# Performance work log

Hardware: AMD Instinct MI355X
Metric: run time of the kernel (lower is better)

Reference implementation:

```python
import jax, jax.numpy as jnp
import numpy as np

NDIM = 128
GDIM = 128
NUM_LAYERS = 2
B = 8192
IDX = 16          # nodes per graph
EPG = 32          # edges per graph
N = B * IDX       # total nodes = 131072
E = B * EPG       # total edges = 262144


def setup_inputs() -> dict:
    key = jax.random.key(0)
    ks = jax.random.split(key, 24)
    h = jax.random.normal(ks[0], (B, IDX, NDIM), dtype=jnp.float32)
    # edges constrained within each graph (flattened node indexing)
    gid = jnp.repeat(jnp.arange(B, dtype=jnp.int64), EPG)
    src = gid * IDX + jax.random.randint(ks[1], (E,), 0, IDX).astype(jnp.int64)
    dst = gid * IDX + jax.random.randint(ks[2], (E,), 0, IDX).astype(jnp.int64)
    edge_index = jnp.stack([src, dst], axis=0)
    s = 0.05
    inp = {
        'h': h,
        'edge_index': edge_index,
        'msg_W': jax.random.normal(ks[3], (NUM_LAYERS, 2 * NDIM, 2 * NDIM), jnp.float32) * s,
        'msg_b': jax.random.normal(ks[4], (NUM_LAYERS, 2 * NDIM), jnp.float32) * s,
        'msgr_W': jax.random.normal(ks[5], (NUM_LAYERS, 2 * NDIM, 2 * NDIM), jnp.float32) * s,
        'msgr_b': jax.random.normal(ks[6], (NUM_LAYERS, 2 * NDIM), jnp.float32) * s,
        'gru_Wih': jax.random.normal(ks[7], (NUM_LAYERS, 3 * NDIM, 2 * NDIM), jnp.float32) * s,
        'gru_Whh': jax.random.normal(ks[8], (NUM_LAYERS, 3 * NDIM, NDIM), jnp.float32) * s,
        'gru_bih': jax.random.normal(ks[9], (NUM_LAYERS, 3 * NDIM), jnp.float32) * s,
        'gru_bhh': jax.random.normal(ks[10], (NUM_LAYERS, 3 * NDIM), jnp.float32) * s,
        'fm_W': jax.random.normal(ks[11], (GDIM, NDIM), jnp.float32) * s,
        'fm_b': jax.random.normal(ks[12], (GDIM,), jnp.float32) * s,
        'gm_W': jax.random.normal(ks[13], (1, NDIM), jnp.float32) * s,
        'gm_b': jax.random.normal(ks[14], (1,), jnp.float32) * s,
        'fmi_W': jax.random.normal(ks[15], (GDIM, NDIM), jnp.float32) * s,
        'fmi_b': jax.random.normal(ks[16], (GDIM,), jnp.float32) * s,
        'gmi_W': jax.random.normal(ks[17], (1, NDIM), jnp.float32) * s,
        'gmi_b': jax.random.normal(ks[18], (1,), jnp.float32) * s,
    }
    return inp


def _gnn_forward(h, edge_index, msg_W, msg_b, msgr_W, msgr_b,
                 gru_Wih, gru_Whh, gru_bih, gru_bhh):
    # h: [N, ndim]; edge_index: [2, E] -> doubled with reversed edges -> [2, 2E]
    ei = jnp.concatenate([edge_index, edge_index[::-1]], axis=1)
    src, dst = ei[0], ei[1]
    e = edge_index.shape[1]
    n_nodes = h.shape[0]
    for l in range(NUM_LAYERS):
        # (eval mode: dropout p=0.0 is a no-op)
        h_j = h[src]                       # [2E, ndim]
        h_i = h[dst]                       # [2E, ndim]
        m = jnp.concatenate([h_j, h_i], axis=1)   # [2E, 2*ndim]
        m_fwd, m_rev = m[:e], m[e:]
        a = jnp.concatenate([
            m_fwd @ msg_W[l].T + msg_b[l],
            m_rev @ msgr_W[l].T + msgr_b[l],
        ], axis=0)                          # [2E, 2*ndim]
        aggr = jax.ops.segment_sum(a, dst, num_segments=n_nodes)  # [N, 2*ndim]
        # GRUCell(aggr, h): gate order r, z, n (torch convention)
        gi = aggr @ gru_Wih[l].T + gru_bih[l]   # [N, 3*ndim]
        gh = h @ gru_Whh[l].T + gru_bhh[l]      # [N, 3*ndim]
        gi_r, gi_z, gi_n = jnp.split(gi, 3, axis=1)
        gh_r, gh_z, gh_n = jnp.split(gh, 3, axis=1)
        r = jax.nn.sigmoid(gi_r + gh_r)
        z = jax.nn.sigmoid(gi_z + gh_z)
        n = jnp.tanh(gi_n + r * gh_n)
        h = n + z * (h - n)                 # (1-z)*n + z*h
    return h


def _graph_aggr(h, idx, f_W, f_b, g_W, g_b):
    # gated sum aggregation
    h_vG = h @ f_W.T + f_b                      # [N, gdim]
    g_vG = jax.nn.sigmoid(h @ g_W.T + g_b)      # [N, 1]
    out = (h_vG * g_vG).reshape(-1, idx, f_W.shape[0])
    return out.sum(axis=1)                      # [B, gdim]


def reference(h, edge_index, msg_W, msg_b, msgr_W, msgr_b,
              gru_Wih, gru_Whh, gru_bih, gru_bhh,
              fm_W, fm_b, gm_W, gm_b, fmi_W, fmi_b, gmi_W, gmi_b):
    idx = h.shape[1]
    hf = h.reshape(-1, NDIM)
    hf = _gnn_forward(hf, edge_index, msg_W, msg_b, msgr_W, msgr_b,
                      gru_Wih, gru_Whh, gru_bih, gru_bhh)
    h_G = _graph_aggr(hf, idx, fm_W, fm_b, gm_W, gm_b)
    h_G_init = _graph_aggr(hf, idx, fmi_W, fmi_b, gmi_W, gmi_b)
    return (hf.reshape(-1, idx, NDIM), h_G, h_G_init)
```

## Files before the change

kernel.cpp:

```cpp
#include <hip/hip_runtime.h>
#include <math.h>
#include <stdint.h>

#define NDIM 128
#define B_GRAPHS 8192
#define IDX 16
#define EPG 32
#define NN (B_GRAPHS*IDX)
#define NE (B_GRAPHS*EPG)

typedef short bf16x8 __attribute__((ext_vector_type(8)));
typedef float f32x4  __attribute__((ext_vector_type(4)));

__device__ inline unsigned short f2bf(float x) {
    union { float f; unsigned u; } v; v.f = x;
    unsigned r = v.u + 0x7fff + ((v.u >> 16) & 1);
    return (unsigned short)(r >> 16);
}
__device__ inline float bf2f(unsigned short b) {
    union { unsigned u; float f; } v; v.u = ((unsigned)b) << 16;
    return v.f;
}
__device__ inline float sigm(float x) { return 1.f/(1.f + __expf(-x)); }
__device__ inline float tanh_f(float x) {
    float ax = fabsf(x);
    float t  = __expf(-2.f*ax);
    float r  = (1.f - t)/(1.f + t);
    return copysignf(r, x);
}

#define GLOAD_LDS16(g, l) \
    __builtin_amdgcn_global_load_lds( \
        (const __attribute__((address_space(1))) unsigned int*)(g), \
        (__attribute__((address_space(3))) unsigned int*)(l), 16, 0, 0)

__global__ __launch_bounds__(256) void compose_kernel(
    const float* __restrict__ msg_W, const float* __restrict__ msgr_W,
    const float* __restrict__ Wih,   const float* __restrict__ Whh,
    const float* __restrict__ msg_b, const float* __restrict__ msgr_b,
    unsigned short* __restrict__ WB, float* __restrict__ c34)
{
    int idx = blockIdx.x*256 + threadIdx.x;
    const int TWB = 2*512*640;
    if (idx < TWB) {
        int l = idx / (512*640); int rem = idx - l*(512*640);
        int cold = rem / 640; int k = rem - cold*640;
        float val;
        if (k < 512) {
            if (cold < 384) {
                const float* wih = Wih + l*384*256 + cold*256;
                const float* M; int sc;
                if (k < 128)      { M = msg_W  + l*256*256; sc = k;       }
                else if (k < 256) { M = msgr_W + l*256*256; sc = k - 128; }
                else if (k < 384) { M = msg_W  + l*256*256; sc = k - 128; }
                else              { M = msgr_W + l*256*256; sc = k - 256; }
                float acc = 0.f;
                for (int q = 0; q < 256; q++) acc = fmaf(wih[q], M[q*256 + sc], acc);
                val = acc;
            } else val = 0.f;
        } else {
            int kk = k - 512;
            if (cold < 256)      val = Whh[l*384*128 + cold*128 + kk];
            else if (cold < 384) val = 0.f;
            else                 val = Whh[l*384*128 + (cold-128)*128 + kk];
        }
        int cc = cold & 127, t = cold >> 7;
        int colp = ((cc >> 4) << 6) + (t << 4) + (cc & 15);
        WB[l*512*640 + colp*640 + k] = f2bf(val);
    } else if (idx < TWB + 2*2*384) {
        int i2 = idx - TWB;
        int l = i2 / 768; int rem = i2 - l*768;
        int which = rem / 384; int r = rem - which*384;
        const float* wih = Wih + l*384*256 + r*256;
        const float* bb  = (which ? msgr_b : msg_b) + l*256;
        float acc = 0.f;
        for (int q = 0; q < 256; q++) acc = fmaf(wih[q], bb[q], acc);
        c34[l*768 + which*384 + r] = acc;
    }
}

__global__ __launch_bounds__(128) void init_kernel(
    const float* __restrict__ hin, const int* __restrict__ ei,
    unsigned short* __restrict__ A, float* __restrict__ indeg,
    float* __restrict__ outdeg, unsigned char* __restrict__ pack)
{
    int g = blockIdx.x, t = threadIdx.x;
    __shared__ float hb[16][128];
    __shared__ float sin_[16][128];
    __shared__ float sout_[16][128];
    __shared__ int sl[32], dl[32];
    __shared__ int cin[16], cout[16];
    __shared__ int flag64;
    int base = g*IDX;
    for (int r = 0; r < 16; r++) hb[r][t] = hin[(size_t)(base+r)*128 + t];
    for (int r = 0; r < 16; r++) { sin_[r][t] = 0.f; sout_[r][t] = 0.f; }
    if (t < 16) { cin[t] = 0; cout[t] = 0; }
    if (t == 0) {
        int orv = 0;
        for (int i = 1; i < 64; i += 2) orv |= ei[i];
        flag64 = (orv == 0);
    }
    __syncthreads();
    if (t < 32) {
        int e = g*EPG + t;
        int sv, dv;
        if (flag64) { sv = ei[2*e]; dv = ei[2*(NE + e)]; }
        else        { sv = ei[e];   dv = ei[NE + e];     }
        sl[t] = sv - base; dl[t] = dv - base;
        atomicAdd(&cout[sl[t]], 1); atomicAdd(&cin[dl[t]], 1);
        pack[g*32 + t] = (unsigned char)((sl[t] & 15) | ((dl[t] & 15) << 4));
    }
    __syncthreads();
    for (int e = 0; e < 32; e++) {
        sin_[dl[e]][t]  += hb[sl[e]][t];
        sout_[sl[e]][t] += hb[dl[e]][t];
    }
    for (int r = 0; r < 16; r++) {
        size_t v = base + r;
        float di = (float)cin[r], dof = (float)cout[r];
        A[v*640 + t]        = f2bf(sin_[r][t]);
        A[v*640 + 128 + t]  = f2bf(sout_[r][t]);
        A[v*640 + 256 + t]  = f2bf(di  * hb[r][t]);
        A[v*640 + 384 + t]  = f2bf(dof * hb[r][t]);
        A[v*640 + 512 + t]  = f2bf(hb[r][t]);
    }
    if (t < 16) { indeg[base+t] = (float)cin[t]; outdeg[base+t] = (float)cout[t]; }
}

struct FSmem {
    unsigned short As[2][64*64];
    union {
        unsigned short Bs[2][384*32];
        unsigned short hnewB[64*128];
    } u;
    unsigned char csr[4][2][17];
    unsigned char adj[4][2][32];
    unsigned char offj[4][2][16];
    float gates[2][64];
};

#define MF(a,b,c) __builtin_amdgcn_mfma_f32_16x16x32_bf16((a),(b),(c),0,0,0)

#define CSTEP(BB, AB, E, J2) do {                                             \
    const unsigned short* Asb = sm.As[AB];                                    \
    const unsigned short* Bsb = sm.u.Bs[BB];                                  \
    bf16x8 bfv[3];                                                            \
    _Pragma("unroll")                                                         \
    for (int tt = 0; tt < 3; tt++) {                                          \
        int a0 = wid*48 + tt*16 + l15;                                        \
        bfv[tt] = *(const bf16x8*)(Bsb + a0*32 + (l4 ^ ((a0>>1)&3))*8);       \
    }                                                                         \
    bf16x8 afv[4];                                                            \
    _Pragma("unroll")                                                         \
    for (int mi = 0; mi < 4; mi++) {                                          \
        int row = mi*16 + l15;                                                \
        int slot = ((E)*4 + l4) ^ (row & 7);                                  \
        afv[mi] = *(const bf16x8*)(Asb + row*64 + slot*8);                    \
    }                                                                         \
    __builtin_amdgcn_s_setprio(1);                                            \
    _Pragma("unroll")                                                         \
    for (int mi = 0; mi < 4; mi++) {                                          \
        acc[mi][0]  = MF(afv[mi], bfv[0], acc[mi][0]);                        \
        acc[mi][1]  = MF(afv[mi], bfv[1], acc[mi][1]);                        \
        acc[mi][J2] = MF(afv[mi], bfv[2], acc[mi][J2]);                       \
    }                                                                         \
    __builtin_amdgcn_s_setprio(0);                                            \
} while (0)

#define WB0 asm volatile("s_waitcnt vmcnt(0)\n\ts_barrier" ::: "memory")
#define WB1 asm volatile("s_waitcnt vmcnt(1)\n\ts_barrier" ::: "memory")

template <bool FINAL>
__global__ __launch_bounds__(512, 4) void fused_kernel(
    unsigned short* __restrict__ A,
    const unsigned short* __restrict__ WBl,
    const unsigned char* __restrict__ pack,
    const float* __restrict__ c34l,
    const float* __restrict__ bihl, const float* __restrict__ bhhl,
    const float* __restrict__ gmW,  const float* __restrict__ gmb,
    const float* __restrict__ gmiW, const float* __restrict__ gmib,
    float* __restrict__ hf, float* __restrict__ P1, float* __restrict__ P2,
    float* __restrict__ sg)
{
    __shared__ FSmem sm;
    const int n0  = blockIdx.x * 64;
    const int g0  = blockIdx.x * 4;
    const int tid = threadIdx.x;
    const int lane = tid & 63, wid = tid >> 6;
    const int l15 = lane & 15, l4 = lane >> 4;

    const int arow = tid >> 3;
    const unsigned short* Abase =
        A + (size_t)(n0 + arow)*640 + (size_t)(((tid & 7) ^ (arow & 7)) * 8);
    int boffv[3], baddv[3];
#pragma unroll
    for (int i = 0; i < 3; i++) {
        int u = i*512 + tid;
        int a = u >> 2, s = u & 3;
        int grp = a / 48, rem = a - grp*48;
        int tt = rem >> 4, clo = rem & 15;
        boffv[i] = (grp*64 + tt*16 + clo)*640 + (s ^ ((a >> 1) & 3))*8;
        baddv[i] = (tt == 2) ? 16*640 : 0;
    }

    auto STAGE_A2 = [&](int p) {
        GLOAD_LDS16(Abase + p*64, sm.As[p & 1] + tid*8);
    };
    auto STAGE_B = [&](int kst) {
        unsigned short* dst = sm.u.Bs[kst & 1] + tid*8;
        const unsigned short* srcb = WBl + kst*32;
        if (kst < 16) {
#pragma unroll
            for (int i = 0; i < 3; i++)
                GLOAD_LDS16(srcb + boffv[i], dst + i*4096);
        } else {
#pragma unroll
            for (int i = 0; i < 3; i++)
                GLOAD_LDS16(srcb + boffv[i] + baddv[i], dst + i*4096);
        }
    };

    STAGE_B(0); STAGE_A2(0);
    if (tid < 8) {
        int gl = tid >> 1, dir = tid & 1;
        const unsigned char* pk = pack + (size_t)(g0 + gl)*32;
        unsigned char* C = sm.csr[gl][dir];
        for (int d = 0; d < 17; d++) C[d] = 0;
        for (int e = 0; e < 32; e++) {
            int p = pk[e];
            int key = dir ? (p & 15) : (p >> 4);
            C[key + 1]++;
        }
        for (int d = 0; d < 16; d++) { C[d+1] += C[d]; sm.offj[gl][dir][d] = C[d]; }
        for (int e = 0; e < 32; e++) {
            int p = pk[e];
            int key = dir ? (p & 15) : (p >> 4);
            int val = dir ? (p >> 4) : (p & 15);
            sm.adj[gl][dir][sm.offj[gl][dir][key]++] = val;
        }
    }

    f32x4 acc[4][4] = {};

    WB0;
    STAGE_B(1);  STAGE_A2(1); CSTEP(0, 0, 0, 2);
    WB1; STAGE_B(2);          CSTEP(1, 0, 1, 2);
    WB0; STAGE_B(3);  STAGE_A2(2); CSTEP(0, 1, 0, 2);
    WB1; STAGE_B(4);          CSTEP(1, 1, 1, 2);
    WB0; STAGE_B(5);  STAGE_A2(3); CSTEP(0, 0, 0, 2);
    WB1; STAGE_B(6);          CSTEP(1, 0, 1, 2);
    WB0; STAGE_B(7);  STAGE_A2(4); CSTEP(0, 1, 0, 2);
    WB1; STAGE_B(8);          CSTEP(1, 1, 1, 2);
    WB0; STAGE_B(9);  STAGE_A2(5); CSTEP(0, 0, 0, 2);
    WB1; STAGE_B(10);         CSTEP(1, 0, 1, 2);
    WB0; STAGE_B(11); STAGE_A2(6); CSTEP(0, 1, 0, 2);
    WB1; STAGE_B(12);         CSTEP(1, 1, 1, 2);
    WB0; STAGE_B(13); STAGE_A2(7); CSTEP(0, 0, 0, 2);
    WB1; STAGE_B(14);         CSTEP(1, 0, 1, 2);
    WB0; STAGE_B(15); STAGE_A2(8); CSTEP(0, 1, 0, 2);
    WB1; STAGE_B(16);         CSTEP(1, 1, 1, 2);
    WB0; STAGE_B(17); STAGE_A2(9); CSTEP(0, 0, 0, 3);
    WB1; STAGE_B(18);         CSTEP(1, 0, 1, 3);
    WB0; STAGE_B(19);         CSTEP(0, 1, 0, 3);
    WB0;                      CSTEP(1, 1, 1, 3);

    {
        const int chn = wid*16 + l15;
        float c3r = c34l[chn],     c3z = c34l[128+chn], c3n = c34l[256+chn];
        float c4r = c34l[384+chn], c4z = c34l[512+chn], c4n = c34l[640+chn];
        float br   = bihl[chn]     + bhhl[chn];
        float bz   = bihl[128+chn] + bhhl[128+chn];
        float bin_ = bihl[256+chn];
        float bhn_ = bhhl[256+chn];
#pragma unroll
        for (int mi = 0; mi < 4; mi++) {
#pragma unroll
            for (int q = 0; q < 4; q++) {
                int row = mi*16 + l4*4 + q;
                size_t v = (size_t)n0 + row;
                int gl = row >> 4, d = row & 15;
                float di  = (float)(sm.csr[gl][0][d+1] - sm.csr[gl][0][d]);
                float dof = (float)(sm.csr[gl][1][d+1] - sm.csr[gl][1][d]);
                float hold = bf2f(A[v*640 + 512 + chn]);
                float rr = sigm(acc[mi][0][q] + di*c3r + dof*c4r + br);
                float zz = sigm(acc[mi][1][q] + di*c3z + dof*c4z + bz);
                float nn = tanh_f(acc[mi][2][q] + di*c3n + dof*c4n + bin_
                                  + rr*(acc[mi][3][q] + bhn_));
                float hv = nn + zz*(hold - nn);
                *(unsigned short*)((char*)sm.u.hnewB
                    + row*256 + ((((chn>>3) ^ (row&7))<<4) + ((chn&7)<<1))) = f2bf(hv);
                if (FINAL) hf[v*128 + chn] = hv;
            }
        }
    }
    __syncthreads();

    if (!FINAL) {
#pragma unroll
        for (int i = 0; i < 10; i++) {
            int u   = i*512 + tid;
            int seg = u >> 10;
            int row = (u >> 4) & 63;
            int c8  = u & 15;
            int gl = row >> 4, d = row & 15;
            float out8[8];
            if (seg < 2) {
#pragma unroll
                for (int k = 0; k < 8; k++) out8[k] = 0.f;
                int e0 = sm.csr[gl][seg][d], e1 = sm.csr[gl][seg][d+1];
                int rb = gl*16;
                for (int j = e0; j < e1; j++) {
                    int r2 = rb + sm.adj[gl][seg][j];
                    bf16x8 v8 = *(const bf16x8*)((const char*)sm.u.hnewB
                                 + r2*256 + ((c8 ^ (r2 & 7)) << 4));
#pragma unroll
                    for (int k = 0; k < 8; k++)
                        out8[k] += bf2f((unsigned short)v8[k]);
                }
            } else {
                bf16x8 v8 = *(const bf16x8*)((const char*)sm.u.hnewB
                             + row*256 + ((c8 ^ (row & 7)) << 4));
                float sc = 1.f;
                if (seg == 2)
                    sc = (float)(sm.csr[gl][0][d+1] - sm.csr[gl][0][d]);
                else if (seg == 3)
                    sc = (float)(sm.csr[gl][1][d+1] - sm.csr[gl][1][d]);
#pragma unroll
                for (int k = 0; k < 8; k++)
                    out8[k] = bf2f((unsigned short)v8[k]) * sc;
            }
            bf16x8 w;
#pragma unroll
            for (int k = 0; k < 8; k++) w[k] = (short)f2bf(out8[k]);
            *(bf16x8*)(A + (size_t)(n0 + row)*640 + seg*128 + c8*8) = w;
        }
    } else {
        if (tid < 64) {
            int row = tid;
            float a1 = 0.f, a2 = 0.f;
            for (int s = 0; s < 16; s++) {
                bf16x8 hv8 = *(const bf16x8*)((const char*)sm.u.hnewB
                              + row*256 + ((s ^ (row & 7)) << 4));
#pragma unroll
                for (int j = 0; j < 8; j++) {
                    float x = bf2f((unsigned short)hv8[j]);
                    int c = s*8 + j;
                    a1 = fmaf(gmW[c],  x, a1);
                    a2 = fmaf(gmiW[c], x, a2);
                }
            }
            sm.gates[0][row] = sigm(a1 + gmb[0]);
            sm.gates[1][row] = sigm(a2 + gmib[0]);
        }
        __syncthreads();
        int c = tid & 127, gq = tid >> 7;
        int rb = gq*16;
        float p1 = 0.f, p2 = 0.f;
        for (int r = 0; r < 16; r++) {
            int rr = rb + r;
            float x = bf2f(*(const unsigned short*)((const char*)sm.u.hnewB
                           + rr*256 + ((((c>>3) ^ (rr&7))<<4) + ((c&7)<<1))));
            p1 = fmaf(sm.gates[0][rr], x, p1);
            p2 = fmaf(sm.gates[1][rr], x, p2);
        }
        size_t g = g0 + gq;
        P1[g*128 + c] = p1;
        P2[g*128 + c] = p2;
        if (tid < 8) {
            int gl = tid >> 1, w = tid & 1;
            float s = 0.f;
            for (int r = 0; r < 16; r++) s += sm.gates[w][gl*16 + r];
            sg[(size_t)(g0 + gl)*2 + w] = s;
        }
    }
}

__global__ __launch_bounds__(256) void outgemm_kernel(
    const float* __restrict__ P1, const float* __restrict__ P2,
    const float* __restrict__ sg,
    const float* __restrict__ fm_W,  const float* __restrict__ fm_b,
    const float* __restrict__ fmi_W, const float* __restrict__ fmi_b,
    float* __restrict__ out1, float* __restrict__ out2)
{
    const int g0 = blockIdx.x * 32;
    const int t  = threadIdx.x;
    __shared__ float Ws[128][33];
    __shared__ float Ps[32][33];
    const int tc = t & 15, tg = t >> 4;

    for (int pass = 0; pass < 2; pass++) {
        const float* P  = pass ? P2 : P1;
        const float* W  = pass ? fmi_W : fm_W;
        const float* bb = pass ? fmi_b : fm_b;
        float acc[2][8] = {};
        for (int kc = 0; kc < 128; kc += 32) {
#pragma unroll
            for (int i = 0; i < 16; i++) {
                int u = i*256 + t; int r = u >> 5, k = u & 31;
                Ws[r][k] = W[(size_t)r*128 + kc + k];
            }
#pragma unroll
            for (int i = 0; i < 4; i++) {
                int u = i*256 + t; int r = u >> 5, k = u & 31;
                Ps[r][k] = P[(size_t)(g0 + r)*128 + kc + k];
            }
            __syncthreads();
#pragma unroll 8
            for (int k = 0; k < 32; k++) {
                float p0 = Ps[tg*2][k], p1v = Ps[tg*2+1][k];
#pragma unroll
                for (int j = 0; j < 8; j++) {
                    float w = Ws[tc*8+j][k];
                    acc[0][j] = fmaf(p0,  w, acc[0][j]);
                    acc[1][j] = fmaf(p1v, w, acc[1][j]);
                }
            }
            __syncthreads();
        }
        float* outp = pass ? out2 : out1;
#pragma unroll
        for (int i = 0; i < 2; i++) {
            int g = g0 + tg*2 + i;
            float sgv = sg[g*2 + pass];
#pragma unroll
            for (int j = 0; j < 8; j++) {
                int cc = tc*8 + j;
                outp[(size_t)g*128 + cc] = acc[i][j] + bb[cc]*sgv;
            }
        }
    }
}

extern "C" void kernel_launch(void* const* d_in, const int* in_sizes, int n_in,
                              void* d_out, int out_size, void* d_ws, size_t ws_size,
                              hipStream_t stream)
{
    const float* h     = (const float*)d_in[0];
    const int*   ei    = (const int*)d_in[1];
    const float* msgW  = (const float*)d_in[2];
    const float* msgb  = (const float*)d_in[3];
    const float* msgrW = (const float*)d_in[4];
    const float* msgrb = (const float*)d_in[5];
    const float* Wih   = (const float*)d_in[6];
    const float* Whh   = (const float*)d_in[7];
    const float* bih   = (const float*)d_in[8];
    const float* bhh   = (const float*)d_in[9];
    const float* fmW   = (const float*)d_in[10];
    const float* fmb   = (const float*)d_in[11];
    const float* gmW   = (const float*)d_in[12];
    const float* gmb   = (const float*)d_in[13];
    const float* fmiW  = (const float*)d_in[14];
    const float* fmib  = (const float*)d_in[15];
    const float* gmiW  = (const float*)d_in[16];
    const float* gmib  = (const float*)d_in[17];

    char* w = (char*)d_ws;
    unsigned short* A    = (unsigned short*)w;  w += (size_t)NN*640*2;
    unsigned short* WB   = (unsigned short*)w;  w += (size_t)2*512*640*2;
    float* c34   = (float*)w;                   w += (size_t)2*768*4;
    float* indeg = (float*)w;                   w += (size_t)NN*4;
    float* outdeg= (float*)w;                   w += (size_t)NN*4;
    unsigned char* pack = (unsigned char*)w;    w += (size_t)B_GRAPHS*32;
    float* P1    = (float*)w;                   w += (size_t)B_GRAPHS*128*4;
    float* P2    = (float*)w;                   w += (size_t)B_GRAPHS*128*4;
    float* sgb   = (float*)w;                   w += (size_t)B_GRAPHS*2*4;

    float* hf   = (float*)d_out;
    float* out1 = hf + (size_t)NN*128;
    float* out2 = out1 + (size_t)B_GRAPHS*128;

    int compose_items = 2*512*640 + 2*2*384;
    compose_kernel<<<(compose_items + 255)/256, 256, 0, stream>>>(
        msgW, msgrW, Wih, Whh, msgb, msgrb, WB, c34);

    init_kernel<<<B_GRAPHS, 128, 0, stream>>>(h, ei, A, indeg, outdeg, pack);

    fused_kernel<false><<<NN/64, 512, 0, stream>>>(
        A, WB, pack, c34, bih, bhh,
        gmW, gmb, gmiW, gmib, nullptr, nullptr, nullptr, nullptr);
    fused_kernel<true><<<NN/64, 512, 0, stream>>>(
        A, WB + (size_t)512*640, pack,
        c34 + 768, bih + 384, bhh + 384,
        gmW, gmb, gmiW, gmib, hf, P1, P2, sgb);

    outgemm_kernel<<<B_GRAPHS/32, 256, 0, stream>>>(
        P1, P2, sgb, fmW, fmb, fmiW, fmib, out1, out2);
}
```

Before: 392.2 us.

## Tile weight composition GEMM, vectorize init stores, read old h from LDS

The naive per-element weight-composition loop moves into a new shared-memory-tiled GEMM kernel, and the original compose kernel now returns early for those elements. The init kernel's feature-row writes become 16-byte bf16x8 vector stores after a barrier, replacing scalar 2-byte stores. The GRU epilogue reads the previous hidden state from the swizzled A tile already staged in LDS instead of reloading it from global memory. Together these cut preprocessing compute and global-memory traffic, at the cost of one extra kernel launch and a dependence on the LDS tile still holding the h columns at the epilogue.

```diff
diff --git a/kernel.cpp b/kernel.cpp
--- a/kernel.cpp
+++ b/kernel.cpp
@@ -33,6 +33,63 @@
     __builtin_amdgcn_global_load_lds( \
         (const __attribute__((address_space(1))) unsigned int*)(g), \
         (__attribute__((address_space(3))) unsigned int*)(l), 16, 0, 0)
+
+__global__ __launch_bounds__(256) void composemm_kernel(
+    const float* __restrict__ msg_W, const float* __restrict__ msgr_W,
+    const float* __restrict__ Wih, unsigned short* __restrict__ WB)
+{
+    int bid = blockIdx.x;
+    int l  = bid / 48; int rem = bid - l*48;
+    int ct = rem >> 3, kt = rem & 7;
+    const int t = threadIdx.x;
+    __shared__ float Ws[64][33];
+    __shared__ float Ms[32][65];
+    const float* wih    = Wih   + (size_t)l*384*256;
+    const float* msgWl  = msg_W + (size_t)l*256*256;
+    const float* msgrWl = msgr_W+ (size_t)l*256*256;
+    float acc[4][4] = {};
+    const int tr  = (t >> 4) * 4;
+    const int tcc = (t & 15) * 4;
+    for (int q0 = 0; q0 < 256; q0 += 32) {
+#pragma unroll
+        for (int i = 0; i < 8; i++) {
+            int u = i*256 + t; int r = u >> 5, q = u & 31;
+            Ws[r][q] = wih[(size_t)(ct*64 + r)*256 + q0 + q];
+        }
+#pragma unroll
+        for (int i = 0; i < 8; i++) {
+            int u = i*256 + t; int q = u >> 6, c = u & 63;
+            int kk = kt*64 + c;
+            int piece = kk >> 7;
+            const float* M = (piece & 1) ? msgrWl : msgWl;
+            int sc = (kk & 127) + ((piece >> 1) << 7);
+            Ms[q][c] = M[(size_t)(q0 + q)*256 + sc];
+        }
+        __syncthreads();
+#pragma unroll 8
+        for (int q = 0; q < 32; q++) {
+#pragma unroll
+            for (int i2 = 0; i2 < 4; i2++) {
+                float wv = Ws[tr + i2][q];
+#pragma unroll
+                for (int j2 = 0; j2 < 4; j2++)
+                    acc[i2][j2] = fmaf(wv, Ms[q][tcc + j2], acc[i2][j2]);
+            }
+        }
+        __syncthreads();
+    }
+#pragma unroll
+    for (int i2 = 0; i2 < 4; i2++) {
+        int cold = ct*64 + tr + i2;
+        int cc = cold & 127, t2 = cold >> 7;
+        int colp = ((cc >> 4) << 6) + (t2 << 4) + (cc & 15);
+#pragma unroll
+        for (int j2 = 0; j2 < 4; j2++) {
+            int k = kt*64 + tcc + j2;
+            WB[(size_t)l*512*640 + (size_t)colp*640 + k] = f2bf(acc[i2][j2]);
+        }
+    }
+}
 
 __global__ __launch_bounds__(256) void compose_kernel(
     const float* __restrict__ msg_W, const float* __restrict__ msgr_W,
@@ -47,17 +104,8 @@
         int cold = rem / 640; int k = rem - cold*640;
         float val;
         if (k < 512) {
-            if (cold < 384) {
-                const float* wih = Wih + l*384*256 + cold*256;
-                const float* M; int sc;
-                if (k < 128)      { M = msg_W  + l*256*256; sc = k;       }
-                else if (k < 256) { M = msgr_W + l*256*256; sc = k - 128; }
-                else if (k < 384) { M = msg_W  + l*256*256; sc = k - 128; }
-                else              { M = msgr_W + l*256*256; sc = k - 256; }
-                float acc = 0.f;
-                for (int q = 0; q < 256; q++) acc = fmaf(wih[q], M[q*256 + sc], acc);
-                val = acc;
-            } else val = 0.f;
+            if (cold < 384) return;
+            val = 0.f;
         } else {
             int kk = k - 512;
             if (cold < 256)      val = Whh[l*384*128 + cold*128 + kk];
@@ -115,14 +163,34 @@
         sin_[dl[e]][t]  += hb[sl[e]][t];
         sout_[sl[e]][t] += hb[dl[e]][t];
     }
-    for (int r = 0; r < 16; r++) {
-        size_t v = base + r;
-        float di = (float)cin[r], dof = (float)cout[r];
-        A[v*640 + t]        = f2bf(sin_[r][t]);
-        A[v*640 + 128 + t]  = f2bf(sout_[r][t]);
-        A[v*640 + 256 + t]  = f2bf(di  * hb[r][t]);
-        A[v*640 + 384 + t]  = f2bf(dof * hb[r][t]);
-        A[v*640 + 512 + t]  = f2bf(hb[r][t]);
+    __syncthreads();
+    {
+        size_t gbase = (size_t)base * 640;
+#pragma unroll
+        for (int i = 0; i < 10; i++) {
+            int u = i*128 + t;
+            int row = u / 80;
+            int j   = u - row*80;
+            int seg = j >> 4;
+            int c0  = (j & 15) * 8;
+            float vals[8];
+            if (seg == 0) {
+#pragma unroll
+                for (int k2 = 0; k2 < 8; k2++) vals[k2] = sin_[row][c0+k2];
+            } else if (seg == 1) {
+#pragma unroll
+                for (int k2 = 0; k2 < 8; k2++) vals[k2] = sout_[row][c0+k2];
+            } else {
+                float s = (seg == 2) ? (float)cin[row]
+                        : (seg == 3) ? (float)cout[row] : 1.f;
+#pragma unroll
+                for (int k2 = 0; k2 < 8; k2++) vals[k2] = hb[row][c0+k2] * s;
+            }
+            bf16x8 w;
+#pragma unroll
+            for (int k2 = 0; k2 < 8; k2++) w[k2] = (short)f2bf(vals[k2]);
+            *(bf16x8*)(A + gbase + (size_t)row*640 + seg*128 + c0) = w;
+        }
     }
     if (t < 16) { indeg[base+t] = (float)cin[t]; outdeg[base+t] = (float)cout[t]; }
 }
@@ -266,6 +334,9 @@
 
     {
         const int chn = wid*16 + l15;
+        const unsigned short* Ah = (chn < 64) ? sm.As[0] : sm.As[1];
+        const int kl = chn & 63;
+        const int klo = ((kl >> 3) << 3);
         float c3r = c34l[chn],     c3z = c34l[128+chn], c3n = c34l[256+chn];
         float c4r = c34l[384+chn], c4z = c34l[512+chn], c4n = c34l[640+chn];
         float br   = bihl[chn]     + bhhl[chn];
@@ -281,7 +352,7 @@
                 int gl = row >> 4, d = row & 15;
                 float di  = (float)(sm.csr[gl][0][d+1] - sm.csr[gl][0][d]);
                 float dof = (float)(sm.csr[gl][1][d+1] - sm.csr[gl][1][d]);
-                float hold = bf2f(A[v*640 + 512 + chn]);
+                float hold = bf2f(Ah[row*64 + (((kl>>3) ^ (row&7))<<3) + (kl&7)]);
                 float rr = sigm(acc[mi][0][q] + di*c3r + dof*c4r + br);
                 float zz = sigm(acc[mi][1][q] + di*c3z + dof*c4z + bz);
                 float nn = tanh_f(acc[mi][2][q] + di*c3n + dof*c4n + bin_
@@ -469,6 +540,7 @@
     float* out1 = hf + (size_t)NN*128;
     float* out2 = out1 + (size_t)B_GRAPHS*128;
 
+    composemm_kernel<<<96, 256, 0, stream>>>(msgW, msgrW, Wih, WB);
     int compose_items = 2*512*640 + 2*2*384;
     compose_kernel<<<(compose_items + 255)/256, 256, 0, stream>>>(
         msgW, msgrW, Wih, Whh, msgb, msgrb, WB, c34);
```

Result: slower. 412.3 us (+5.1%).
